# Optimization experiments

Measured on AMD Instinct MI355X. Metric: run time of the kernel, lower is better.

The kernel has to match this reference:

```python
import jax, jax.numpy as jnp
import numpy as np

N_NODES = 100000
N_HEDGES = 30000
N_PINS = 400000
D = 128          # hidden_channels
H = 4            # heads
K = D // H       # per-head dim
N_BLOCKS = 4     # n_layers=2, each layer = (vertex2edge, edge2vertex)
LN_EPS = 1e-5


def setup_inputs() -> dict:
    key = jax.random.key(0)
    ks = jax.random.split(key, 10)
    s = 1.0 / np.sqrt(D)
    return {
        "x_0": jax.random.normal(ks[0], (N_NODES, D), jnp.float32),
        "Kw": jax.random.normal(ks[1], (N_BLOCKS, H, D, K), jnp.float32) * s,
        "Vw": jax.random.normal(ks[2], (N_BLOCKS, H, D, K), jnp.float32) * s,
        "Qw": jax.random.normal(ks[3], (N_BLOCKS, H, K), jnp.float32) * s,
        "W1": jax.random.normal(ks[4], (N_BLOCKS, D, D), jnp.float32) * s,
        "b1": jnp.zeros((N_BLOCKS, D), jnp.float32),
        "W2": jax.random.normal(ks[5], (N_BLOCKS, D, D), jnp.float32) * s,
        "b2": jnp.zeros((N_BLOCKS, D), jnp.float32),
        "ln0_g": jnp.ones((N_BLOCKS, D), jnp.float32),
        "ln0_b": jnp.zeros((N_BLOCKS, D), jnp.float32),
        "ln1_g": jnp.ones((N_BLOCKS, D), jnp.float32),
        "ln1_b": jnp.zeros((N_BLOCKS, D), jnp.float32),
        "node_idx": jax.random.randint(ks[6], (N_PINS,), 0, N_NODES),
        "hedge_idx": jax.random.randint(ks[7], (N_PINS,), 0, N_HEDGES),
        "n_hyperedges": N_HEDGES,
    }


def _ln(x, g, b):
    mu = jnp.mean(x, -1, keepdims=True)
    var = jnp.mean((x - mu) ** 2, -1, keepdims=True)
    return (x - mu) * jax.lax.rsqrt(var + LN_EPS) * g + b


def _segment_softmax(logits, seg, num_segments):
    # softmax over incident pins grouped by target (sparse softmax over source dim)
    m = jax.ops.segment_max(logits, seg, num_segments=num_segments)
    ex = jnp.exp(logits - m[seg])
    denom = jax.ops.segment_sum(ex, seg, num_segments=num_segments)
    return ex / denom[seg]


def _block(x_src, src, tgt, n_tgt, Kw, Vw, Qw, W1, b1, W2, b2, g0, be0, g1, be1):
    # Multi-head PMA attention with a single learned query per head.
    Kx = jnp.einsum('nd,hdk->nhk', x_src, Kw)           # [n_src, H, K]
    Vx = jnp.einsum('nd,hdk->nhk', x_src, Vw)           # [n_src, H, K]
    logits = jnp.einsum('hk,nhk->nh', Qw, Kx)           # [n_src, H]
    w = _segment_softmax(logits[src], tgt, n_tgt)       # [E, H]
    msg = (w[:, :, None] * Vx[src]).reshape(-1, H * K)  # [E, D] head-concat
    agg = jax.ops.segment_sum(msg, tgt, num_segments=n_tgt)  # [n_tgt, D]
    x = _ln(agg + Qw.reshape(1, H * K), g0, be0)        # Q skip + LN0
    h = jnp.maximum(x @ W1 + b1, 0.0) @ W2 + b2         # 2-layer MLP
    return _ln(x + h, g1, be1)                          # residual + LN1


def reference(x_0, Kw, Vw, Qw, W1, b1, W2, b2, ln0_g, ln0_b, ln1_g, ln1_b,
              node_idx, hedge_idx, n_hyperedges):
    n_nodes = x_0.shape[0]
    x0, x1 = x_0, None
    for layer in range(N_BLOCKS // 2):
        bv, bev = 2 * layer, 2 * layer + 1
        # vertex -> hyperedge
        x1 = jax.nn.relu(_block(x0, node_idx, hedge_idx, n_hyperedges,
                                Kw[bv], Vw[bv], Qw[bv], W1[bv], b1[bv], W2[bv], b2[bv],
                                ln0_g[bv], ln0_b[bv], ln1_g[bv], ln1_b[bv]))
        # hyperedge -> vertex
        x0 = jax.nn.relu(_block(x1, hedge_idx, node_idx, n_nodes,
                                Kw[bev], Vw[bev], Qw[bev], W1[bev], b1[bev], W2[bev], b2[bev],
                                ln0_g[bev], ln0_b[bev], ln1_g[bev], ln1_b[bev]))
    return (x0, x1)
```

## Files before the change

### kernel.cpp

```cpp
#include <hip/hip_runtime.h>

#define N_NODES 100000
#define N_HEDGES 30000
#define N_PINS 400000
#define NPN 100096
#define NPH 30080
#define OVF_CAP 8192
#define SCAN_BH 118
#define SCAN_BN 391

typedef __attribute__((ext_vector_type(8))) short bf16x8;
typedef __attribute__((ext_vector_type(4))) float f32x4;
typedef unsigned short ushort_t;

__device__ __forceinline__ unsigned short f2bf(float f) {
  unsigned int u = __float_as_uint(f);
  u += 0x7FFF + ((u >> 16) & 1);
  return (unsigned short)(u >> 16);
}
__device__ __forceinline__ float bf2f(unsigned short s) {
  return __uint_as_float(((unsigned int)s) << 16);
}
__device__ __forceinline__ void gload16(const void* g, void* l) {
  __builtin_amdgcn_global_load_lds(
      (const __attribute__((address_space(1))) unsigned int*)g,
      (__attribute__((address_space(3))) unsigned int*)l, 16, 0, 0);
}

__global__ __launch_bounds__(256) void fused_front(
    const float* __restrict__ x0_in, ushort_t* __restrict__ x0b,
    const int* __restrict__ node_idx, const int* __restrict__ hedge_idx,
    int* __restrict__ cntN, int* __restrict__ cntH, unsigned* __restrict__ rank2,
    const float* __restrict__ Kw, const float* __restrict__ Vw,
    const float* __restrict__ Qw, const float* __restrict__ W1,
    const float* __restrict__ W2, ushort_t* __restrict__ Vvqsw,
    ushort_t* __restrict__ W1sw, ushort_t* __restrict__ W2sw) {
  int gsz = gridDim.x * 256;
  int tid = blockIdx.x * 256 + threadIdx.x;
  int rn = 0, rh = 0;
  bool hasPin = tid < N_PINS;
  if (hasPin) {
    int n_i = node_idx[tid], h_i = hedge_idx[tid];
    rn = atomicAdd(&cntN[n_i], 1);
    rh = atomicAdd(&cntH[h_i], 1);
  }
  for (int i = tid; i < N_NODES * 16; i += gsz) {
    const float4* s = (const float4*)x0_in + (size_t)i * 2;
    float4 a = s[0], b = s[1];
    uint4 o;
    o.x = ((unsigned)f2bf(a.y) << 16) | f2bf(a.x);
    o.y = ((unsigned)f2bf(a.w) << 16) | f2bf(a.z);
    o.z = ((unsigned)f2bf(b.y) << 16) | f2bf(b.x);
    o.w = ((unsigned)f2bf(b.w) << 16) | f2bf(b.z);
    ((uint4*)x0b)[i] = o;
  }
  for (int i = tid; i < 4 * 144 * 128; i += gsz) {
    int b = i / 18432, r = i % 18432, c = r >> 7, d = r & 127;
    float v;
    if (c < 128) {
      v = Vw[((b * 4 + (c >> 5)) * 128 + d) * 32 + (c & 31)];
    } else if (c < 132) {
      int h = c - 128;
      const float* kp = Kw + ((b * 4 + h) * 128 + d) * 32;
      const float* qp = Qw + (b * 4 + h) * 32;
      float s = 0.f;
      for (int k = 0; k < 32; ++k) s += kp[k] * qp[k];
      v = s;
    } else {
      v = 0.f;
    }
    int L = (c * 256 + d * 2) ^ ((c & 7) << 4);
    Vvqsw[b * 18432 + L / 2] = f2bf(v);
  }
  for (int i = tid; i < 4 * 128 * 128; i += gsz) {
    int b = i >> 14, r = i & 16383, c = r >> 7, k = r & 127;
    int L = (c * 256 + k * 2) ^ ((c & 7) << 4);
    int idx = b * 16384 + L / 2;
    W1sw[idx] = f2bf(W1[b * 16384 + k * 128 + c]);
    W2sw[idx] = f2bf(W2[b * 16384 + k * 128 + c]);
  }
  if (hasPin) rank2[tid] = ((unsigned)rh << 16) | (unsigned)rn;
}

__global__ __launch_bounds__(256) void csr_scan2(
    const int* __restrict__ cntH, int2* __restrict__ segH, int* __restrict__ ovfH,
    const int* __restrict__ cntN, int2* __restrict__ segN, int* __restrict__ ovfN,
    int* __restrict__ gctr) {
  __shared__ int wsum[4];
  __shared__ int bbase;
  bool isH = (int)blockIdx.x < SCAN_BH;
  const int* cnt = isH ? cntH : cntN;
  int2* seg = isH ? segH : segN;
  int* ovf = isH ? ovfH : ovfN;
  int* g = gctr + (isH ? 0 : 1);
  int* oc = gctr + (isH ? 2 : 3);
  int thresh = isH ? 32 : 16;
  int n = isH ? N_HEDGES : N_NODES;
  int i = (isH ? (int)blockIdx.x : (int)blockIdx.x - SCAN_BH) * 256 + threadIdx.x;
  int lane = threadIdx.x & 63, wid = threadIdx.x >> 6;
  int v = (i < n) ? cnt[i] : 0;
  int sc = v;
#pragma unroll
  for (int s = 1; s < 64; s <<= 1) {
    int tv = __shfl_up(sc, s);
    if (lane >= s) sc += tv;
  }
  if (lane == 63) wsum[wid] = sc;
  __syncthreads();
  if (threadIdx.x == 0) {
    int s0 = wsum[0], s1 = wsum[1], s2 = wsum[2], s3 = wsum[3];
    wsum[0] = 0; wsum[1] = s0; wsum[2] = s0 + s1; wsum[3] = s0 + s1 + s2;
    bbase = atomicAdd(g, s0 + s1 + s2 + s3);
  }
  __syncthreads();
  if (i < n) {
    int st = bbase + wsum[wid] + (sc - v);
    seg[i] = make_int2(st, v);
    if (v > thresh) {
      int k = atomicAdd(oc, 1);
      if (k < OVF_CAP) ovf[k] = i;
    }
  }
}

__global__ __launch_bounds__(256) void csr_fill(
    const int* __restrict__ node_idx, const int* __restrict__ hedge_idx,
    const unsigned* __restrict__ rank2, const int2* __restrict__ segN,
    const int2* __restrict__ segH, int* __restrict__ pinsN,
    int* __restrict__ pinsH) {
  int e = blockIdx.x * 256 + threadIdx.x;
  if (e < N_PINS) {
    int n = node_idx[e], h = hedge_idx[e];
    unsigned r2 = rank2[e];
    pinsH[segH[h].x + (int)(r2 >> 16)] = n;
    pinsN[segN[n].x + (int)(r2 & 0xffffu)] = h;
  }
}

__global__ __launch_bounds__(256) void transform_k(
    const ushort_t* __restrict__ xb, const ushort_t* __restrict__ Bsw,
    ushort_t* __restrict__ Vxb, float* __restrict__ lg, int n) {
  __shared__ char Blds[36864];
  __shared__ char Olds[16384];
  int t = threadIdx.x, l = t & 63, w = t >> 6;
  size_t r0 = (size_t)blockIdx.x * 64;
#pragma unroll
  for (int it = 0; it < 9; ++it) {
    int off = it * 4096 + w * 1024 + l * 16;
    gload16((const char*)Bsw + off, Blds + off);
  }
  __syncthreads();

  f32x4 acc[9];
#pragma unroll
  for (int ct = 0; ct < 9; ++ct) acc[ct] = (f32x4){0.f, 0.f, 0.f, 0.f};
  int swz = (l & 7) << 4;
  int lbase = (l & 15) * 256 + (l >> 4) * 16;
  const ushort_t* abase = xb + (r0 + w * 16 + (l & 15)) * 128 + (l >> 4) * 8;
#pragma unroll
  for (int kk = 0; kk < 4; ++kk) {
    bf16x8 a = *(const bf16x8*)(abase + kk * 32);
#pragma unroll
    for (int ct = 0; ct < 9; ++ct) {
      bf16x8 b = *(const bf16x8*)(Blds + ((ct * 4096 + kk * 64 + lbase) ^ swz));
      acc[ct] = __builtin_amdgcn_mfma_f32_16x16x32_bf16(a, b, acc[ct], 0, 0, 0);
    }
  }
  if ((l & 15) < 4) {
    size_t rb = r0 + w * 16 + (l >> 4) * 4;
#pragma unroll
    for (int j = 0; j < 4; ++j) lg[(rb + j) * 4 + (l & 15)] = acc[8][j];
  }
  int row64 = w * 16 + (l >> 4) * 4;
#pragma unroll
  for (int ct = 0; ct < 8; ++ct) {
    int c2 = (ct * 16 + (l & 15)) * 2;
#pragma unroll
    for (int j = 0; j < 4; ++j) {
      int r = row64 + j;
      int addr = (r * 256 + c2) ^ ((r & 0xC) << 3);
      *(ushort_t*)(Olds + addr) = f2bf(acc[ct][j]);
    }
  }
  __syncthreads();
#pragma unroll
  for (int it = 0; it < 4; ++it) {
    int L = it * 4096 + t * 16;
    int r = L >> 8;
    int phys = L ^ ((r & 0xC) << 3);
    *(uint4*)((char*)Vxb + r0 * 256 + L) = *(const uint4*)(Olds + phys);
  }
}

template <int L>
__global__ __launch_bounds__(256) void attn_g(
    const ushort_t* __restrict__ Vxb, const float* __restrict__ lg,
    const int2* __restrict__ seg, const int* __restrict__ pins,
    const float* __restrict__ Qflat, const float* __restrict__ g0,
    const float* __restrict__ be0, ushort_t* __restrict__ xmidb, int n_tgt,
    int mainBlocks, const int* __restrict__ ovf, const int* __restrict__ ovfcnt) {
  constexpr int G = 64 / L;
  constexpr int C = 128 / L;
  __shared__ float wl[4][G][L][4];
  __shared__ int pl[4][G][L];
  int wid = threadIdx.x >> 6, lane = threadIdx.x & 63;
  const char* vb = (const char*)Vxb;

  if ((int)blockIdx.x < mainBlocks) {
    int g = lane / L, li = lane % L;
    int tg = ((int)blockIdx.x * 4 + wid) * G + g;
    bool tval = tg < n_tgt;
    int2 sc = tval ? seg[tg] : make_int2(0, 0);
    int base = sc.x, deg = sc.y;
    bool fast = deg <= L;
    int mydeg = (tval && fast) ? deg : 0;
    bool act = li < mydeg;
    int p = act ? pins[base + li] : 0;
    float4 l4;
    if (act) l4 = *(const float4*)(lg + p * 4);
    else l4 = make_float4(-3.4e38f, -3.4e38f, -3.4e38f, -3.4e38f);
    float m0 = l4.x, m1 = l4.y, m2 = l4.z, m3 = l4.w;
#pragma unroll
    for (int off = 1; off < L; off <<= 1) {
      m0 = fmaxf(m0, __shfl_xor(m0, off));
      m1 = fmaxf(m1, __shfl_xor(m1, off));
      m2 = fmaxf(m2, __shfl_xor(m2, off));
      m3 = fmaxf(m3, __shfl_xor(m3, off));
    }
    float e0 = __expf(l4.x - m0), e1 = __expf(l4.y - m1);
    float e2 = __expf(l4.z - m2), e3 = __expf(l4.w - m3);
    float s0 = e0, s1 = e1, s2 = e2, s3 = e3;
#pragma unroll
    for (int off = 1; off < L; off <<= 1) {
      s0 += __shfl_xor(s0, off);
      s1 += __shfl_xor(s1, off);
      s2 += __shfl_xor(s2, off);
      s3 += __shfl_xor(s3, off);
    }
    wl[wid][g][li][0] = e0 / s0;
    wl[wid][g][li][1] = e1 / s1;
    wl[wid][g][li][2] = e2 / s2;
    wl[wid][g][li][3] = e3 / s3;
    pl[wid][g][li] = p << 8;

    int myh = li / (L / 4);
    float acc[C];
#pragma unroll
    for (int c = 0; c < C; ++c) acc[c] = 0.f;
    for (int e = 0; e < mydeg; ++e) {
      int off = pl[wid][g][e];
      float wgt = wl[wid][g][e][myh];
      const char* src = vb + off + li * (C * 2);
      unsigned u[C / 2];
      if constexpr (C == 8) {
        uint4 v = *(const uint4*)src;
        u[0] = v.x; u[1] = v.y; u[2] = v.z; u[3] = v.w;
      } else {
        uint2 v = *(const uint2*)src;
        u[0] = v.x; u[1] = v.y;
      }
#pragma unroll
      for (int j = 0; j < C / 2; ++j) {
        acc[2 * j] = fmaf(wgt, __uint_as_float(u[j] << 16), acc[2 * j]);
        acc[2 * j + 1] = fmaf(wgt, __uint_as_float(u[j] & 0xffff0000u), acc[2 * j + 1]);
      }
    }
    float q[C], gv[C], bv[C];
#pragma unroll
    for (int j = 0; j < C / 4; ++j) {
      float4 t = *(const float4*)(Qflat + li * C + j * 4);
      q[j * 4] = t.x; q[j * 4 + 1] = t.y; q[j * 4 + 2] = t.z; q[j * 4 + 3] = t.w;
      t = *(const float4*)(g0 + li * C + j * 4);
      gv[j * 4] = t.x; gv[j * 4 + 1] = t.y; gv[j * 4 + 2] = t.z; gv[j * 4 + 3] = t.w;
      t = *(const float4*)(be0 + li * C + j * 4);
      bv[j * 4] = t.x; bv[j * 4 + 1] = t.y; bv[j * 4 + 2] = t.z; bv[j * 4 + 3] = t.w;
    }
    float t1 = 0.f, t2 = 0.f;
#pragma unroll
    for (int c = 0; c < C; ++c) {
      float x = acc[c] + q[c];
      acc[c] = x;
      t1 += x;
      t2 += x * x;
    }
#pragma unroll
    for (int off = 1; off < L; off <<= 1) {
      t1 += __shfl_xor(t1, off);
      t2 += __shfl_xor(t2, off);
    }
    float mean = t1 * (1.f / 128.f);
    float var = t2 * (1.f / 128.f) - mean * mean;
    float rs = rsqrtf(var + 1e-5f);
    if (tval && fast) {
      float o[C];
#pragma unroll
      for (int c = 0; c < C; ++c) o[c] = (acc[c] - mean) * rs * gv[c] + bv[c];
      char* dst = (char*)xmidb + (size_t)tg * 256 + li * (C * 2);
      if constexpr (C == 8) {
        uint4 pk;
        pk.x = ((unsigned)f2bf(o[1]) << 16) | f2bf(o[0]);
        pk.y = ((unsigned)f2bf(o[3]) << 16) | f2bf(o[2]);
        pk.z = ((unsigned)f2bf(o[5]) << 16) | f2bf(o[4]);
        pk.w = ((unsigned)f2bf(o[7]) << 16) | f2bf(o[6]);
        *(uint4*)dst = pk;
      } else {
        uint2 pk;
        pk.x = ((unsigned)f2bf(o[1]) << 16) | f2bf(o[0]);
        pk.y = ((unsigned)f2bf(o[3]) << 16) | f2bf(o[2]);
        *(uint2*)dst = pk;
      }
    }
    return;
  }

  int cnt = *ovfcnt;
  if (cnt > OVF_CAP) cnt = OVF_CAP;
  int head = lane >> 4;
  for (int idx = ((int)blockIdx.x - mainBlocks) * 4 + wid; idx < cnt; idx += 128) {
    int tg = ovf[idx];
    int2 sc = seg[tg];
    int base = sc.x, deg = sc.y;
    float m0 = -3.4e38f, m1 = -3.4e38f, m2 = -3.4e38f, m3 = -3.4e38f;
    for (int i = lane; i < deg; i += 64) {
      int p = pins[base + i];
      float4 l4 = *(const float4*)(lg + p * 4);
      m0 = fmaxf(m0, l4.x); m1 = fmaxf(m1, l4.y);
      m2 = fmaxf(m2, l4.z); m3 = fmaxf(m3, l4.w);
    }
#pragma unroll
    for (int off = 1; off < 64; off <<= 1) {
      m0 = fmaxf(m0, __shfl_xor(m0, off));
      m1 = fmaxf(m1, __shfl_xor(m1, off));
      m2 = fmaxf(m2, __shfl_xor(m2, off));
      m3 = fmaxf(m3, __shfl_xor(m3, off));
    }
    float s0 = 0.f, s1 = 0.f, s2 = 0.f, s3 = 0.f;
    for (int i = lane; i < deg; i += 64) {
      int p = pins[base + i];
      float4 l4 = *(const float4*)(lg + p * 4);
      s0 += __expf(l4.x - m0); s1 += __expf(l4.y - m1);
      s2 += __expf(l4.z - m2); s3 += __expf(l4.w - m3);
    }
#pragma unroll
    for (int off = 1; off < 64; off <<= 1) {
      s0 += __shfl_xor(s0, off);
      s1 += __shfl_xor(s1, off);
      s2 += __shfl_xor(s2, off);
      s3 += __shfl_xor(s3, off);
    }
    float mh = (head & 2) ? ((head & 1) ? m3 : m2) : ((head & 1) ? m1 : m0);
    float sh = (head & 2) ? ((head & 1) ? s3 : s2) : ((head & 1) ? s1 : s0);
    float rdh = (deg > 0) ? 1.f / sh : 0.f;
    float acc0 = 0.f, acc1 = 0.f;
    for (int e = 0; e < deg; ++e) {
      int p = pins[base + e];
      float w0 = __expf(lg[p * 4 + head] - mh) * rdh;
      unsigned int v = *(const unsigned int*)(vb + (p << 8) + lane * 4);
      acc0 = fmaf(w0, __uint_as_float(v << 16), acc0);
      acc1 = fmaf(w0, __uint_as_float(v & 0xffff0000u), acc1);
    }
    float2 q2 = ((const float2*)Qflat)[lane];
    float x0v = acc0 + q2.x;
    float x1v = acc1 + q2.y;
    float t1 = x0v + x1v, t2 = x0v * x0v + x1v * x1v;
#pragma unroll
    for (int off = 1; off < 64; off <<= 1) {
      t1 += __shfl_xor(t1, off);
      t2 += __shfl_xor(t2, off);
    }
    float mean = t1 * (1.f / 128.f);
    float var = t2 * (1.f / 128.f) - mean * mean;
    float rs = rsqrtf(var + 1e-5f);
    float2 gg = ((const float2*)g0)[lane];
    float2 bb = ((const float2*)be0)[lane];
    float o0 = (x0v - mean) * rs * gg.x + bb.x;
    float o1 = (x1v - mean) * rs * gg.y + bb.y;
    unsigned int pk = ((unsigned int)f2bf(o1) << 16) | f2bf(o0);
    ((unsigned int*)xmidb)[tg * 64 + lane] = pk;
  }
}

__global__ __launch_bounds__(256) void mlp_k(
    const ushort_t* __restrict__ xmb, const ushort_t* __restrict__ W1sw,
    const float* __restrict__ b1, const ushort_t* __restrict__ W2sw,
    const float* __restrict__ b2, const float* __restrict__ g1,
    const float* __restrict__ be1, float* __restrict__ outf,
    ushort_t* __restrict__ outb, int n, int flags) {
  __shared__ char Wlds[32768];
  __shared__ char Hlds[16384];
  int t = threadIdx.x, l = t & 63, w = t >> 6;
  size_t r0 = (size_t)blockIdx.x * 64;
#pragma unroll
  for (int it = 0; it < 8; ++it) {
    int off = it * 4096 + w * 1024 + l * 16;
    gload16((const char*)W1sw + off, Wlds + off);
  }
  float b1v[8], b2v[8], g1v[8], be1v[8];
#pragma unroll
  for (int ct = 0; ct < 8; ++ct) {
    int c = ct * 16 + (l & 15);
    b1v[ct] = b1[c]; b2v[ct] = b2[c]; g1v[ct] = g1[c]; be1v[ct] = be1[c];
  }
  __syncthreads();

  int swz = (l & 7) << 4;
  int lbase = (l & 15) * 256 + (l >> 4) * 16;
  f32x4 acc[8];
#pragma unroll
  for (int ct = 0; ct < 8; ++ct) acc[ct] = (f32x4){b1v[ct], b1v[ct], b1v[ct], b1v[ct]};
  const ushort_t* abase = xmb + (r0 + w * 16 + (l & 15)) * 128 + (l >> 4) * 8;
#pragma unroll
  for (int kk = 0; kk < 4; ++kk) {
    bf16x8 a = *(const bf16x8*)(abase + kk * 32);
#pragma unroll
    for (int ct = 0; ct < 8; ++ct) {
      bf16x8 b = *(const bf16x8*)(Wlds + ((ct * 4096 + kk * 64 + lbase) ^ swz));
      acc[ct] = __builtin_amdgcn_mfma_f32_16x16x32_bf16(a, b, acc[ct], 0, 0, 0);
    }
  }
  int hbase = w * 4096;
#pragma unroll
  for (int ct = 0; ct < 8; ++ct) {
    int c2 = (ct * 16 + (l & 15)) * 2;
#pragma unroll
    for (int j = 0; j < 4; ++j) {
      int rl = (l >> 4) * 4 + j;
      int addr = hbase + ((rl * 256 + c2) ^ ((rl & 7) << 4));
      *(ushort_t*)(Hlds + addr) = f2bf(fmaxf(acc[ct][j], 0.f));
    }
  }
  __syncthreads();
#pragma unroll
  for (int it = 0; it < 8; ++it) {
    int off = it * 4096 + w * 1024 + l * 16;
    gload16((const char*)W2sw + off, Wlds + off);
  }
  __syncthreads();

  f32x4 acc2[8];
#pragma unroll
  for (int ct = 0; ct < 8; ++ct) acc2[ct] = (f32x4){b2v[ct], b2v[ct], b2v[ct], b2v[ct]};
#pragma unroll
  for (int kk = 0; kk < 4; ++kk) {
    bf16x8 a = *(const bf16x8*)(Hlds + (hbase + ((lbase + kk * 64) ^ swz)));
#pragma unroll
    for (int ct = 0; ct < 8; ++ct) {
      bf16x8 b = *(const bf16x8*)(Wlds + ((ct * 4096 + kk * 64 + lbase) ^ swz));
      acc2[ct] = __builtin_amdgcn_mfma_f32_16x16x32_bf16(a, b, acc2[ct], 0, 0, 0);
    }
  }
  size_t rbase = r0 + w * 16 + (l >> 4) * 4;
  float s1[4] = {0.f, 0.f, 0.f, 0.f}, s2[4] = {0.f, 0.f, 0.f, 0.f};
#pragma unroll
  for (int ct = 0; ct < 8; ++ct) {
    int c = ct * 16 + (l & 15);
#pragma unroll
    for (int j = 0; j < 4; ++j) {
      float x = bf2f(xmb[(rbase + j) * 128 + c]);
      float y = acc2[ct][j] + x;
      acc2[ct][j] = y;
      s1[j] += y;
      s2[j] += y * y;
    }
  }
#pragma unroll
  for (int off = 1; off < 16; off <<= 1) {
#pragma unroll
    for (int j = 0; j < 4; ++j) {
      s1[j] += __shfl_xor(s1[j], off);
      s2[j] += __shfl_xor(s2[j], off);
    }
  }
  float mean[4], rs[4];
#pragma unroll
  for (int j = 0; j < 4; ++j) {
    mean[j] = s1[j] * (1.f / 128.f);
    float var = s2[j] * (1.f / 128.f) - mean[j] * mean[j];
    rs[j] = rsqrtf(var + 1e-5f);
  }
#pragma unroll
  for (int ct = 0; ct < 8; ++ct) {
    int c = ct * 16 + (l & 15);
#pragma unroll
    for (int j = 0; j < 4; ++j) {
      float o = fmaxf((acc2[ct][j] - mean[j]) * rs[j] * g1v[ct] + be1v[ct], 0.f);
      size_t row = rbase + j;
      if (flags & 2) outb[row * 128 + c] = f2bf(o);
      if ((flags & 1) && row < (size_t)n) outf[row * 128 + c] = o;
    }
  }
}

extern "C" void kernel_launch(void* const* d_in, const int* in_sizes, int n_in,
                              void* d_out, int out_size, void* d_ws, size_t ws_size,
                              hipStream_t stream) {
  const float* x0_in = (const float*)d_in[0];
  const float* Kw  = (const float*)d_in[1];
  const float* Vw  = (const float*)d_in[2];
  const float* Qw  = (const float*)d_in[3];
  const float* W1  = (const float*)d_in[4];
  const float* b1  = (const float*)d_in[5];
  const float* W2  = (const float*)d_in[6];
  const float* b2  = (const float*)d_in[7];
  const float* ln0g = (const float*)d_in[8];
  const float* ln0b = (const float*)d_in[9];
  const float* ln1g = (const float*)d_in[10];
  const float* ln1b = (const float*)d_in[11];
  const int* node_idx  = (const int*)d_in[12];
  const int* hedge_idx = (const int*)d_in[13];

  float* out = (float*)d_out;
  float* x0_out = out;
  float* x1_out = out + (size_t)N_NODES * 128;

  char* w = (char*)d_ws;
  auto alloc = [&](size_t bytes) -> void* {
    void* p = (void*)w;
    w += (bytes + 255) & ~(size_t)255;
    return p;
  };
  ushort_t* Vvqsw = (ushort_t*)alloc(4 * 18432 * 2);
  ushort_t* W1sw  = (ushort_t*)alloc(4 * 16384 * 2);
  ushort_t* W2sw  = (ushort_t*)alloc(4 * 16384 * 2);
  ushort_t* x0b   = (ushort_t*)alloc((size_t)NPN * 128 * 2);
  ushort_t* x1b   = (ushort_t*)alloc((size_t)NPH * 128 * 2);
  ushort_t* Vxb   = (ushort_t*)alloc((size_t)NPN * 128 * 2);
  float*    lg    = (float*)alloc((size_t)NPN * 4 * 4);
  ushort_t* xmidb = (ushort_t*)alloc((size_t)NPN * 128 * 2);
  int2* segH  = (int2*)alloc((size_t)N_HEDGES * 8);
  int2* segN  = (int2*)alloc((size_t)N_NODES * 8);
  int* pinsH  = (int*)alloc(N_PINS * 4);
  int* pinsN  = (int*)alloc(N_PINS * 4);
  int* ovfH   = (int*)alloc(OVF_CAP * 4);
  int* ovfN   = (int*)alloc(OVF_CAP * 4);
  unsigned* rank2 = (unsigned*)alloc((size_t)N_PINS * 4);
  int* zbase  = (int*)alloc((size_t)(N_HEDGES + N_NODES + 4) * 4);
  int* cntH = zbase;
  int* cntN = cntH + N_HEDGES;
  int* gctr = cntN + N_NODES;

  hipMemsetAsync(zbase, 0, (size_t)(N_HEDGES + N_NODES + 4) * 4, stream);

  fused_front<<<2048, 256, 0, stream>>>(x0_in, x0b, node_idx, hedge_idx, cntN, cntH,
                                        rank2, Kw, Vw, Qw, W1, W2, Vvqsw, W1sw, W2sw);
  csr_scan2<<<SCAN_BH + SCAN_BN, 256, 0, stream>>>(cntH, segH, ovfH,
                                                   cntN, segN, ovfN, gctr);
  csr_fill<<<(N_PINS + 255) / 256, 256, 0, stream>>>(node_idx, hedge_idx, rank2,
                                                     segN, segH, pinsN, pinsH);

  const ushort_t* srcs[4] = {x0b, x1b, x0b, x1b};
  int n_srcs[4] = {N_NODES, N_HEDGES, N_NODES, N_HEDGES};
  const int2* segs[4] = {segH, segN, segH, segN};
  const int* pinss[4] = {pinsH, pinsN, pinsH, pinsN};
  int n_tgts[4] = {N_HEDGES, N_NODES, N_HEDGES, N_NODES};
  float* outf[4] = {x1_out, x0_out, x1_out, x0_out};
  ushort_t* outbs[4] = {x1b, x0b, x1b, x0b};
  int flags[4] = {2, 2, 3, 1};

  const int mbH = (N_HEDGES + 7) / 8;
  const int mbN = (N_NODES + 15) / 16;

  for (int b = 0; b < 4; ++b) {
    int n_src = n_srcs[b], n_tgt = n_tgts[b];
    transform_k<<<(n_src + 63) / 64, 256, 0, stream>>>(srcs[b], Vvqsw + b * 18432,
                                                       Vxb, lg, n_src);
    if (b & 1) {
      attn_g<16><<<mbN + 32, 256, 0, stream>>>(Vxb, lg, segs[b], pinss[b],
                                               Qw + b * 128, ln0g + b * 128,
                                               ln0b + b * 128, xmidb, n_tgt,
                                               mbN, ovfN, gctr + 3);
    } else {
      attn_g<32><<<mbH + 32, 256, 0, stream>>>(Vxb, lg, segs[b], pinss[b],
                                               Qw + b * 128, ln0g + b * 128,
                                               ln0b + b * 128, xmidb, n_tgt,
                                               mbH, ovfH, gctr + 2);
    }
    mlp_k<<<(n_tgt + 63) / 64, 256, 0, stream>>>(xmidb, W1sw + b * 16384, b1 + b * 128,
                                                 W2sw + b * 16384, b2 + b * 128,
                                                 ln1g + b * 128, ln1b + b * 128,
                                                 outf[b], outbs[b], n_tgt, flags[b]);
  }
}
```

Baseline: 287.8 us.

## Fuse next block's V/logit transform into MLP epilogue and CSR scan

Removes the standalone transform kernel. The first block's transform runs as extra blocks inside the CSR scan launch. Each later block's transform is computed in the previous MLP's epilogue from the LayerNorm output held in LDS. This drops four launches and the bf16 round trip of the intermediate node/hyperedge features through global memory. The MLP tile also grows to 128 rows per block with 64 KB of shared memory, which can lower occupancy and raise register pressure.

```diff
diff --git a/kernel.cpp b/kernel.cpp
--- a/kernel.cpp
+++ b/kernel.cpp
@@ -4,10 +4,11 @@
 #define N_HEDGES 30000
 #define N_PINS 400000
 #define NPN 100096
-#define NPH 30080
 #define OVF_CAP 8192
 #define SCAN_BH 118
 #define SCAN_BN 391
+#define SCAN_B (SCAN_BH + SCAN_BN)
+#define TB 1563
 
 typedef __attribute__((ext_vector_type(8))) short bf16x8;
 typedef __attribute__((ext_vector_type(4))) float f32x4;
@@ -82,44 +83,101 @@
   if (hasPin) rank2[tid] = ((unsigned)rh << 16) | (unsigned)rn;
 }
 
-__global__ __launch_bounds__(256) void csr_scan2(
+__global__ __launch_bounds__(256) void scan_tf(
     const int* __restrict__ cntH, int2* __restrict__ segH, int* __restrict__ ovfH,
     const int* __restrict__ cntN, int2* __restrict__ segN, int* __restrict__ ovfN,
-    int* __restrict__ gctr) {
+    int* __restrict__ gctr, const ushort_t* __restrict__ xb,
+    const ushort_t* __restrict__ Bsw, ushort_t* __restrict__ Vxb,
+    float* __restrict__ lg) {
+  __shared__ char Blds[36864];
+  __shared__ char Olds[16384];
   __shared__ int wsum[4];
   __shared__ int bbase;
-  bool isH = (int)blockIdx.x < SCAN_BH;
-  const int* cnt = isH ? cntH : cntN;
-  int2* seg = isH ? segH : segN;
-  int* ovf = isH ? ovfH : ovfN;
-  int* g = gctr + (isH ? 0 : 1);
-  int* oc = gctr + (isH ? 2 : 3);
-  int thresh = isH ? 32 : 16;
-  int n = isH ? N_HEDGES : N_NODES;
-  int i = (isH ? (int)blockIdx.x : (int)blockIdx.x - SCAN_BH) * 256 + threadIdx.x;
-  int lane = threadIdx.x & 63, wid = threadIdx.x >> 6;
-  int v = (i < n) ? cnt[i] : 0;
-  int sc = v;
-#pragma unroll
-  for (int s = 1; s < 64; s <<= 1) {
-    int tv = __shfl_up(sc, s);
-    if (lane >= s) sc += tv;
-  }
-  if (lane == 63) wsum[wid] = sc;
-  __syncthreads();
-  if (threadIdx.x == 0) {
-    int s0 = wsum[0], s1 = wsum[1], s2 = wsum[2], s3 = wsum[3];
-    wsum[0] = 0; wsum[1] = s0; wsum[2] = s0 + s1; wsum[3] = s0 + s1 + s2;
-    bbase = atomicAdd(g, s0 + s1 + s2 + s3);
-  }
-  __syncthreads();
-  if (i < n) {
-    int st = bbase + wsum[wid] + (sc - v);
-    seg[i] = make_int2(st, v);
-    if (v > thresh) {
-      int k = atomicAdd(oc, 1);
-      if (k < OVF_CAP) ovf[k] = i;
-    }
+  int t = threadIdx.x, l = t & 63, w = t >> 6;
+
+  if ((int)blockIdx.x < SCAN_B) {
+    bool isH = (int)blockIdx.x < SCAN_BH;
+    const int* cnt = isH ? cntH : cntN;
+    int2* seg = isH ? segH : segN;
+    int* ovf = isH ? ovfH : ovfN;
+    int* g = gctr + (isH ? 0 : 1);
+    int* oc = gctr + (isH ? 2 : 3);
+    int thresh = isH ? 32 : 16;
+    int n = isH ? N_HEDGES : N_NODES;
+    int i = (isH ? (int)blockIdx.x : (int)blockIdx.x - SCAN_BH) * 256 + t;
+    int lane = t & 63, wid = t >> 6;
+    int v = (i < n) ? cnt[i] : 0;
+    int sc = v;
+#pragma unroll
+    for (int s = 1; s < 64; s <<= 1) {
+      int tv = __shfl_up(sc, s);
+      if (lane >= s) sc += tv;
+    }
+    if (lane == 63) wsum[wid] = sc;
+    __syncthreads();
+    if (t == 0) {
+      int s0 = wsum[0], s1 = wsum[1], s2 = wsum[2], s3 = wsum[3];
+      wsum[0] = 0; wsum[1] = s0; wsum[2] = s0 + s1; wsum[3] = s0 + s1 + s2;
+      bbase = atomicAdd(g, s0 + s1 + s2 + s3);
+    }
+    __syncthreads();
+    if (i < n) {
+      int st = bbase + wsum[wid] + (sc - v);
+      seg[i] = make_int2(st, v);
+      if (v > thresh) {
+        int k = atomicAdd(oc, 1);
+        if (k < OVF_CAP) ovf[k] = i;
+      }
+    }
+    return;
+  }
+
+  size_t r0 = (size_t)((int)blockIdx.x - SCAN_B) * 64;
+#pragma unroll
+  for (int it = 0; it < 9; ++it) {
+    int off = it * 4096 + w * 1024 + l * 16;
+    gload16((const char*)Bsw + off, Blds + off);
+  }
+  __syncthreads();
+
+  f32x4 acc[9];
+#pragma unroll
+  for (int ct = 0; ct < 9; ++ct) acc[ct] = (f32x4){0.f, 0.f, 0.f, 0.f};
+  int swz = (l & 7) << 4;
+  int lbase = (l & 15) * 256 + (l >> 4) * 16;
+  const ushort_t* abase = xb + (r0 + w * 16 + (l & 15)) * 128 + (l >> 4) * 8;
+#pragma unroll
+  for (int kk = 0; kk < 4; ++kk) {
+    bf16x8 a = *(const bf16x8*)(abase + kk * 32);
+#pragma unroll
+    for (int ct = 0; ct < 9; ++ct) {
+      bf16x8 b = *(const bf16x8*)(Blds + ((ct * 4096 + kk * 64 + lbase) ^ swz));
+      acc[ct] = __builtin_amdgcn_mfma_f32_16x16x32_bf16(a, b, acc[ct], 0, 0, 0);
+    }
+  }
+  if ((l & 15) < 4) {
+    size_t rb = r0 + w * 16 + (l >> 4) * 4;
+#pragma unroll
+    for (int j = 0; j < 4; ++j) lg[(rb + j) * 4 + (l & 15)] = acc[8][j];
+  }
+  int row64 = w * 16 + (l >> 4) * 4;
+#pragma unroll
+  for (int ct = 0; ct < 8; ++ct) {
+    int c2 = (ct * 16 + (l & 15)) * 2;
+#pragma unroll
+    for (int j = 0; j < 4; ++j) {
+      int r = row64 + j;
+      int addr = (r * 256 + c2) ^ ((r & 0xC) << 3);
+      *(ushort_t*)(Olds + addr) = f2bf(acc[ct][j]);
+    }
+  }
+  __syncthreads();
+#pragma unroll
+  for (int it = 0; it < 4; ++it) {
+    int L = it * 4096 + t * 16;
+    int r = L >> 8;
+    int phys = L ^ ((r & 0xC) << 3);
+    *(uint4*)((char*)Vxb + r0 * 256 + L) = *(const uint4*)(Olds + phys);
   }
 }
 
@@ -134,61 +192,6 @@
     unsigned r2 = rank2[e];
     pinsH[segH[h].x + (int)(r2 >> 16)] = n;
     pinsN[segN[n].x + (int)(r2 & 0xffffu)] = h;
-  }
-}
-
-__global__ __launch_bounds__(256) void transform_k(
-    const ushort_t* __restrict__ xb, const ushort_t* __restrict__ Bsw,
-    ushort_t* __restrict__ Vxb, float* __restrict__ lg, int n) {
-  __shared__ char Blds[36864];
-  __shared__ char Olds[16384];
-  int t = threadIdx.x, l = t & 63, w = t >> 6;
-  size_t r0 = (size_t)blockIdx.x * 64;
-#pragma unroll
-  for (int it = 0; it < 9; ++it) {
-    int off = it * 4096 + w * 1024 + l * 16;
-    gload16((const char*)Bsw + off, Blds + off);
-  }
-  __syncthreads();
-
-  f32x4 acc[9];
-#pragma unroll
-  for (int ct = 0; ct < 9; ++ct) acc[ct] = (f32x4){0.f, 0.f, 0.f, 0.f};
-  int swz = (l & 7) << 4;
-  int lbase = (l & 15) * 256 + (l >> 4) * 16;
-  const ushort_t* abase = xb + (r0 + w * 16 + (l & 15)) * 128 + (l >> 4) * 8;
-#pragma unroll
-  for (int kk = 0; kk < 4; ++kk) {
-    bf16x8 a = *(const bf16x8*)(abase + kk * 32);
-#pragma unroll
-    for (int ct = 0; ct < 9; ++ct) {
-      bf16x8 b = *(const bf16x8*)(Blds + ((ct * 4096 + kk * 64 + lbase) ^ swz));
-      acc[ct] = __builtin_amdgcn_mfma_f32_16x16x32_bf16(a, b, acc[ct], 0, 0, 0);
-    }
-  }
-  if ((l & 15) < 4) {
-    size_t rb = r0 + w * 16 + (l >> 4) * 4;
-#pragma unroll
-    for (int j = 0; j < 4; ++j) lg[(rb + j) * 4 + (l & 15)] = acc[8][j];
-  }
-  int row64 = w * 16 + (l >> 4) * 4;
-#pragma unroll
-  for (int ct = 0; ct < 8; ++ct) {
-    int c2 = (ct * 16 + (l & 15)) * 2;
-#pragma unroll
-    for (int j = 0; j < 4; ++j) {
-      int r = row64 + j;
-      int addr = (r * 256 + c2) ^ ((r & 0xC) << 3);
-      *(ushort_t*)(Olds + addr) = f2bf(acc[ct][j]);
-    }
-  }
-  __syncthreads();
-#pragma unroll
-  for (int it = 0; it < 4; ++it) {
-    int L = it * 4096 + t * 16;
-    int r = L >> 8;
-    int phys = L ^ ((r & 0xC) << 3);
-    *(uint4*)((char*)Vxb + r0 * 256 + L) = *(const uint4*)(Olds + phys);
   }
 }
 
@@ -380,16 +383,23 @@
   }
 }
 
-__global__ __launch_bounds__(256) void mlp_k(
+__global__ __launch_bounds__(256) void mlp128(
     const ushort_t* __restrict__ xmb, const ushort_t* __restrict__ W1sw,
     const float* __restrict__ b1, const ushort_t* __restrict__ W2sw,
     const float* __restrict__ b2, const float* __restrict__ g1,
-    const float* __restrict__ be1, float* __restrict__ outf,
-    ushort_t* __restrict__ outb, int n, int flags) {
-  __shared__ char Wlds[32768];
-  __shared__ char Hlds[16384];
+    const float* __restrict__ be1, float* __restrict__ outf, int n, int wf32,
+    const ushort_t* __restrict__ Bsw, ushort_t* __restrict__ Vxb,
+    float* __restrict__ lg) {
+  __shared__ char S[65536];
+  char* Wlds = S;
+  char* HX = S + 32768;
   int t = threadIdx.x, l = t & 63, w = t >> 6;
-  size_t r0 = (size_t)blockIdx.x * 64;
+  size_t r0 = (size_t)blockIdx.x * 128;
+  int rb = w * 32;
+  int swz = (l & 7) << 4;
+  int lbase = (l & 15) * 256 + (l >> 4) * 16;
+  bool do_tf = (Bsw != nullptr);
+
 #pragma unroll
   for (int it = 0; it < 8; ++it) {
     int off = it * 4096 + w * 1024 + l * 16;
@@ -403,30 +413,34 @@
   }
   __syncthreads();
 
-  int swz = (l & 7) << 4;
-  int lbase = (l & 15) * 256 + (l >> 4) * 16;
-  f32x4 acc[8];
-#pragma unroll
-  for (int ct = 0; ct < 8; ++ct) acc[ct] = (f32x4){b1v[ct], b1v[ct], b1v[ct], b1v[ct]};
-  const ushort_t* abase = xmb + (r0 + w * 16 + (l & 15)) * 128 + (l >> 4) * 8;
+  f32x4 acc0[8], acc1[8];
+#pragma unroll
+  for (int ct = 0; ct < 8; ++ct) {
+    acc0[ct] = (f32x4){b1v[ct], b1v[ct], b1v[ct], b1v[ct]};
+    acc1[ct] = (f32x4){b1v[ct], b1v[ct], b1v[ct], b1v[ct]};
+  }
+  const ushort_t* a0p = xmb + (r0 + rb + (l & 15)) * 128 + (l >> 4) * 8;
+  const ushort_t* a1p = a0p + 16 * 128;
 #pragma unroll
   for (int kk = 0; kk < 4; ++kk) {
-    bf16x8 a = *(const bf16x8*)(abase + kk * 32);
+    bf16x8 a0 = *(const bf16x8*)(a0p + kk * 32);
+    bf16x8 a1 = *(const bf16x8*)(a1p + kk * 32);
 #pragma unroll
     for (int ct = 0; ct < 8; ++ct) {
       bf16x8 b = *(const bf16x8*)(Wlds + ((ct * 4096 + kk * 64 + lbase) ^ swz));
-      acc[ct] = __builtin_amdgcn_mfma_f32_16x16x32_bf16(a, b, acc[ct], 0, 0, 0);
-    }
-  }
-  int hbase = w * 4096;
+      acc0[ct] = __builtin_amdgcn_mfma_f32_16x16x32_bf16(a0, b, acc0[ct], 0, 0, 0);
+      acc1[ct] = __builtin_amdgcn_mfma_f32_16x16x32_bf16(a1, b, acc1[ct], 0, 0, 0);
+    }
+  }
 #pragma unroll
   for (int ct = 0; ct < 8; ++ct) {
     int c2 = (ct * 16 + (l & 15)) * 2;
 #pragma unroll
     for (int j = 0; j < 4; ++j) {
-      int rl = (l >> 4) * 4 + j;
-      int addr = hbase + ((rl * 256 + c2) ^ ((rl & 7) << 4));
-      *(ushort_t*)(Hlds + addr) = f2bf(fmaxf(acc[ct][j], 0.f));
+      int rl0 = rb + (l >> 4) * 4 + j;
+      int rl1 = rl0 + 16;
+      *(ushort_t*)(HX + ((rl0 * 256 + c2) ^ ((rl0 & 7) << 4))) = f2bf(fmaxf(acc0[ct][j], 0.f));
+      *(ushort_t*)(HX + ((rl1 * 256 + c2) ^ ((rl1 & 7) << 4))) = f2bf(fmaxf(acc1[ct][j], 0.f));
     }
   }
   __syncthreads();
@@ -437,57 +451,139 @@
   }
   __syncthreads();
 
-  f32x4 acc2[8];
-#pragma unroll
-  for (int ct = 0; ct < 8; ++ct) acc2[ct] = (f32x4){b2v[ct], b2v[ct], b2v[ct], b2v[ct]};
+  f32x4 ac20[8], ac21[8];
+#pragma unroll
+  for (int ct = 0; ct < 8; ++ct) {
+    ac20[ct] = (f32x4){b2v[ct], b2v[ct], b2v[ct], b2v[ct]};
+    ac21[ct] = (f32x4){b2v[ct], b2v[ct], b2v[ct], b2v[ct]};
+  }
+  int h0base = (rb + (l & 15)) * 256;
+  int h1base = h0base + 16 * 256;
 #pragma unroll
   for (int kk = 0; kk < 4; ++kk) {
-    bf16x8 a = *(const bf16x8*)(Hlds + (hbase + ((lbase + kk * 64) ^ swz)));
+    bf16x8 a0 = *(const bf16x8*)(HX + h0base + (((l >> 4) * 16 + kk * 64) ^ swz));
+    bf16x8 a1 = *(const bf16x8*)(HX + h1base + (((l >> 4) * 16 + kk * 64) ^ swz));
 #pragma unroll
     for (int ct = 0; ct < 8; ++ct) {
       bf16x8 b = *(const bf16x8*)(Wlds + ((ct * 4096 + kk * 64 + lbase) ^ swz));
-      acc2[ct] = __builtin_amdgcn_mfma_f32_16x16x32_bf16(a, b, acc2[ct], 0, 0, 0);
-    }
-  }
-  size_t rbase = r0 + w * 16 + (l >> 4) * 4;
-  float s1[4] = {0.f, 0.f, 0.f, 0.f}, s2[4] = {0.f, 0.f, 0.f, 0.f};
+      ac20[ct] = __builtin_amdgcn_mfma_f32_16x16x32_bf16(a0, b, ac20[ct], 0, 0, 0);
+      ac21[ct] = __builtin_amdgcn_mfma_f32_16x16x32_bf16(a1, b, ac21[ct], 0, 0, 0);
+    }
+  }
+  size_t rbase0 = r0 + rb + (l >> 4) * 4;
+  size_t rbase1 = rbase0 + 16;
+  float s10[4] = {0, 0, 0, 0}, s20[4] = {0, 0, 0, 0};
+  float s11[4] = {0, 0, 0, 0}, s21[4] = {0, 0, 0, 0};
 #pragma unroll
   for (int ct = 0; ct < 8; ++ct) {
     int c = ct * 16 + (l & 15);
 #pragma unroll
     for (int j = 0; j < 4; ++j) {
-      float x = bf2f(xmb[(rbase + j) * 128 + c]);
-      float y = acc2[ct][j] + x;
-      acc2[ct][j] = y;
-      s1[j] += y;
-      s2[j] += y * y;
+      float x0 = bf2f(xmb[(rbase0 + j) * 128 + c]);
+      float y0 = ac20[ct][j] + x0;
+      ac20[ct][j] = y0; s10[j] += y0; s20[j] += y0 * y0;
+      float x1 = bf2f(xmb[(rbase1 + j) * 128 + c]);
+      float y1 = ac21[ct][j] + x1;
+      ac21[ct][j] = y1; s11[j] += y1; s21[j] += y1 * y1;
     }
   }
 #pragma unroll
   for (int off = 1; off < 16; off <<= 1) {
 #pragma unroll
     for (int j = 0; j < 4; ++j) {
-      s1[j] += __shfl_xor(s1[j], off);
-      s2[j] += __shfl_xor(s2[j], off);
-    }
-  }
-  float mean[4], rs[4];
+      s10[j] += __shfl_xor(s10[j], off);
+      s20[j] += __shfl_xor(s20[j], off);
+      s11[j] += __shfl_xor(s11[j], off);
+      s21[j] += __shfl_xor(s21[j], off);
+    }
+  }
+  float mean0[4], rs0[4], mean1[4], rs1[4];
 #pragma unroll
   for (int j = 0; j < 4; ++j) {
-    mean[j] = s1[j] * (1.f / 128.f);
-    float var = s2[j] * (1.f / 128.f) - mean[j] * mean[j];
-    rs[j] = rsqrtf(var + 1e-5f);
+    mean0[j] = s10[j] * (1.f / 128.f);
+    rs0[j] = rsqrtf(s20[j] * (1.f / 128.f) - mean0[j] * mean0[j] + 1e-5f);
+    mean1[j] = s11[j] * (1.f / 128.f);
+    rs1[j] = rsqrtf(s21[j] * (1.f / 128.f) - mean1[j] * mean1[j] + 1e-5f);
   }
 #pragma unroll
   for (int ct = 0; ct < 8; ++ct) {
     int c = ct * 16 + (l & 15);
+    int c2 = c * 2;
 #pragma unroll
     for (int j = 0; j < 4; ++j) {
-      float o = fmaxf((acc2[ct][j] - mean[j]) * rs[j] * g1v[ct] + be1v[ct], 0.f);
-      size_t row = rbase + j;
-      if (flags & 2) outb[row * 128 + c] = f2bf(o);
-      if ((flags & 1) && row < (size_t)n) outf[row * 128 + c] = o;
-    }
+      float o0 = fmaxf((ac20[ct][j] - mean0[j]) * rs0[j] * g1v[ct] + be1v[ct], 0.f);
+      float o1 = fmaxf((ac21[ct][j] - mean1[j]) * rs1[j] * g1v[ct] + be1v[ct], 0.f);
+      int rl0 = rb + (l >> 4) * 4 + j;
+      int rl1 = rl0 + 16;
+      if (do_tf) {
+        *(ushort_t*)(HX + ((rl0 * 256 + c2) ^ ((rl0 & 7) << 4))) = f2bf(o0);
+        *(ushort_t*)(HX + ((rl1 * 256 + c2) ^ ((rl1 & 7) << 4))) = f2bf(o1);
+      }
+      if (wf32) {
+        size_t row0 = rbase0 + j, row1 = rbase1 + j;
+        if (row0 < (size_t)n) outf[row0 * 128 + c] = o0;
+        if (row1 < (size_t)n) outf[row1 * 128 + c] = o1;
+      }
+    }
+  }
+  if (!do_tf) return;
+  __syncthreads();
+
+  char* Blds = S;
+#pragma unroll
+  for (int it = 0; it < 8; ++it) {
+    int off = it * 4096 + w * 1024 + l * 16;
+    gload16((const char*)Bsw + off, Blds + off);
+  }
+  __syncthreads();
+
+  f32x4 ta0[9], ta1[9];
+#pragma unroll
+  for (int ct = 0; ct < 9; ++ct) {
+    ta0[ct] = (f32x4){0.f, 0.f, 0.f, 0.f};
+    ta1[ct] = (f32x4){0.f, 0.f, 0.f, 0.f};
+  }
+#pragma unroll
+  for (int kk = 0; kk < 4; ++kk) {
+    bf16x8 a0 = *(const bf16x8*)(HX + h0base + (((l >> 4) * 16 + kk * 64) ^ swz));
+    bf16x8 a1 = *(const bf16x8*)(HX + h1base + (((l >> 4) * 16 + kk * 64) ^ swz));
+#pragma unroll
+    for (int ct = 0; ct < 8; ++ct) {
+      bf16x8 b = *(const bf16x8*)(Blds + ((ct * 4096 + kk * 64 + lbase) ^ swz));
+      ta0[ct] = __builtin_amdgcn_mfma_f32_16x16x32_bf16(a0, b, ta0[ct], 0, 0, 0);
+      ta1[ct] = __builtin_amdgcn_mfma_f32_16x16x32_bf16(a1, b, ta1[ct], 0, 0, 0);
+    }
+    bf16x8 bq = *(const bf16x8*)((const char*)Bsw + 32768 + ((kk * 64 + lbase) ^ swz));
+    ta0[8] = __builtin_amdgcn_mfma_f32_16x16x32_bf16(a0, bq, ta0[8], 0, 0, 0);
+    ta1[8] = __builtin_amdgcn_mfma_f32_16x16x32_bf16(a1, bq, ta1[8], 0, 0, 0);
+  }
+  if ((l & 15) < 4) {
+#pragma unroll
+    for (int j = 0; j < 4; ++j) {
+      lg[(rbase0 + j) * 4 + (l & 15)] = ta0[8][j];
+      lg[(rbase1 + j) * 4 + (l & 15)] = ta1[8][j];
+    }
+  }
+  __syncthreads();
+  char* Olds = HX;
+#pragma unroll
+  for (int ct = 0; ct < 8; ++ct) {
+    int c2 = (ct * 16 + (l & 15)) * 2;
+#pragma unroll
+    for (int j = 0; j < 4; ++j) {
+      int rr0 = rb + (l >> 4) * 4 + j;
+      int rr1 = rr0 + 16;
+      *(ushort_t*)(Olds + ((rr0 * 256 + c2) ^ ((rr0 & 0xC) << 3))) = f2bf(ta0[ct][j]);
+      *(ushort_t*)(Olds + ((rr1 * 256 + c2) ^ ((rr1 & 0xC) << 3))) = f2bf(ta1[ct][j]);
+    }
+  }
+  __syncthreads();
+#pragma unroll
+  for (int it = 0; it < 8; ++it) {
+    int L = it * 4096 + t * 16;
+    int r = L >> 8;
+    int phys = L ^ ((r & 0xC) << 3);
+    *(uint4*)((char*)Vxb + r0 * 256 + L) = *(const uint4*)(Olds + phys);
   }
 }
 
@@ -523,7 +619,6 @@
   ushort_t* W1sw  = (ushort_t*)alloc(4 * 16384 * 2);
   ushort_t* W2sw  = (ushort_t*)alloc(4 * 16384 * 2);
   ushort_t* x0b   = (ushort_t*)alloc((size_t)NPN * 128 * 2);
-  ushort_t* x1b   = (ushort_t*)alloc((size_t)NPH * 128 * 2);
   ushort_t* Vxb   = (ushort_t*)alloc((size_t)NPN * 128 * 2);
   float*    lg    = (float*)alloc((size_t)NPN * 4 * 4);
   ushort_t* xmidb = (ushort_t*)alloc((size_t)NPN * 128 * 2);
@@ -543,27 +638,19 @@
 
   fused_front<<<2048, 256, 0, stream>>>(x0_in, x0b, node_idx, hedge_idx, cntN, cntH,
                                         rank2, Kw, Vw, Qw, W1, W2, Vvqsw, W1sw, W2sw);
-  csr_scan2<<<SCAN_BH + SCAN_BN, 256, 0, stream>>>(cntH, segH, ovfH,
-                                                   cntN, segN, ovfN, gctr);
+  scan_tf<<<SCAN_B + TB, 256, 0, stream>>>(cntH, segH, ovfH, cntN, segN, ovfN,
+                                           gctr, x0b, Vvqsw, Vxb, lg);
   csr_fill<<<(N_PINS + 255) / 256, 256, 0, stream>>>(node_idx, hedge_idx, rank2,
                                                      segN, segH, pinsN, pinsH);
 
-  const ushort_t* srcs[4] = {x0b, x1b, x0b, x1b};
-  int n_srcs[4] = {N_NODES, N_HEDGES, N_NODES, N_HEDGES};
   const int2* segs[4] = {segH, segN, segH, segN};
   const int* pinss[4] = {pinsH, pinsN, pinsH, pinsN};
   int n_tgts[4] = {N_HEDGES, N_NODES, N_HEDGES, N_NODES};
-  float* outf[4] = {x1_out, x0_out, x1_out, x0_out};
-  ushort_t* outbs[4] = {x1b, x0b, x1b, x0b};
-  int flags[4] = {2, 2, 3, 1};
-
   const int mbH = (N_HEDGES + 7) / 8;
   const int mbN = (N_NODES + 15) / 16;
 
   for (int b = 0; b < 4; ++b) {
-    int n_src = n_srcs[b], n_tgt = n_tgts[b];
-    transform_k<<<(n_src + 63) / 64, 256, 0, stream>>>(srcs[b], Vvqsw + b * 18432,
-                                                       Vxb, lg, n_src);
+    int n_tgt = n_tgts[b];
     if (b & 1) {
       attn_g<16><<<mbN + 32, 256, 0, stream>>>(Vxb, lg, segs[b], pinss[b],
                                                Qw + b * 128, ln0g + b * 128,
@@ -575,9 +662,19 @@
                                                ln0b + b * 128, xmidb, n_tgt,
                                                mbH, ovfH, gctr + 2);
     }
-    mlp_k<<<(n_tgt + 63) / 64, 256, 0, stream>>>(xmidb, W1sw + b * 16384, b1 + b * 128,
-                                                 W2sw + b * 16384, b2 + b * 128,
-                                                 ln1g + b * 128, ln1b + b * 128,
-                                                 outf[b], outbs[b], n_tgt, flags[b]);
-  }
-}
+    int nblk = (n_tgt + 127) / 128;
+    if (b < 3) {
+      int wf32 = (b == 2) ? 1 : 0;
+      float* of = (b == 2) ? x1_out : nullptr;
+      mlp128<<<nblk, 256, 0, stream>>>(
+          xmidb, W1sw + b * 16384, b1 + b * 128, W2sw + b * 16384, b2 + b * 128,
+          ln1g + b * 128, ln1b + b * 128, of, n_tgt, wf32,
+          Vvqsw + (b + 1) * 18432, Vxb, lg);
+    } else {
+      mlp128<<<nblk, 256, 0, stream>>>(
+          xmidb, W1sw + b * 16384, b1 + b * 128, W2sw + b * 16384, b2 + b * 128,
+          ln1g + b * 128, ln1b + b * 128, x0_out, n_tgt, 1,
+          nullptr, nullptr, nullptr);
+    }
+  }
+}
```

Result: slower. 306.4 us (+6.5%).
